# Kernel tuning notes

Measured on AMD Instinct MI355X. Metric: run time of the kernel, lower is better.

## Reference

```python
import jax, jax.numpy as jnp
import numpy as np
import math

B, T, H = 16, 2048, 128

def setup_inputs() -> dict:
    key = jax.random.key(0)
    kq, kk, kv = jax.random.split(key, 3)
    q = jax.random.normal(kq, (B, T, H), dtype=jnp.float32)
    k = jax.random.normal(kk, (B, T, H), dtype=jnp.float32)
    v = jax.random.normal(kv, (B, T, H), dtype=jnp.float32)
    # causal mask, shape (1,1,T,T) as in the torch module
    mask = jnp.tril(jnp.ones((T, T), dtype=jnp.int32))[None, None]
    return {"q": q, "k": k, "v": v, "mask": mask}

def reference(q, k, v, mask) -> jnp.ndarray:
    scale = math.sqrt(q.shape[-1])
    # (B,T,T) attention logits
    att = jnp.einsum("btd,bsd->bts", q, k) / scale
    m = mask[0, 0]  # (T,T), broadcasts over batch
    att = jnp.where(m == 0, -jnp.inf, att)
    att = jax.nn.softmax(att, axis=-1)
    # dropout is identity in eval mode (p=0.0)
    return jnp.einsum("bts,bsd->btd", att, v)
```

## Files before the change

kernel.cpp:

```cpp
#include <hip/hip_runtime.h>
#include <hip/hip_bf16.h>

#define TT 2048
#define DD 128
#define NB 16
#define NTILE 32
#define TILE_BYTES 16384

typedef __bf16 bf16x8 __attribute__((ext_vector_type(8)));
typedef __bf16 bf16x4 __attribute__((ext_vector_type(4)));
typedef float f32x4 __attribute__((ext_vector_type(4)));
typedef float f32x16 __attribute__((ext_vector_type(16)));

#define GLOAD_LDS16(g, l) __builtin_amdgcn_global_load_lds( \
    (const __attribute__((address_space(1))) void*)(g),     \
    (__attribute__((address_space(3))) void*)(l), 16, 0, 0)

__device__ __forceinline__ float warp16_sum(float v) {
    v += __shfl_xor(v, 1);
    v += __shfl_xor(v, 2);
    v += __shfl_xor(v, 4);
    v += __shfl_xor(v, 8);
    return v;
}
__device__ __forceinline__ float bf2f(unsigned int u16) {
    union { unsigned int i; float f; } x; x.i = u16 << 16; return x.f;
}
__device__ __forceinline__ unsigned int pk2(float lo, float hi) {
    unsigned short a = __builtin_bit_cast(unsigned short, (__bf16)lo);
    unsigned short b = __builtin_bit_cast(unsigned short, (__bf16)hi);
    return (unsigned int)a | ((unsigned int)b << 16);
}
__device__ __forceinline__ bf16x8 frag4(unsigned int a, unsigned int b,
                                        unsigned int c, unsigned int d) {
    uint4 u = make_uint4(a, b, c, d);
    return __builtin_bit_cast(bf16x8, u);
}
__device__ __forceinline__ f32x16 z16() {
    f32x16 v;
    #pragma unroll
    for (int i = 0; i < 16; ++i) v[i] = 0.f;
    return v;
}

__global__ __launch_bounds__(256) void prepass(
    const float* __restrict__ K, const float* __restrict__ V,
    char* __restrict__ KB, char* __restrict__ VTB)
{
    const int t = blockIdx.x;
    const int b = blockIdx.y;
    const int tid = threadIdx.x;
    char* kdst = KB  + (size_t)(b * NTILE + t) * TILE_BYTES;
    char* vdst = VTB + (size_t)(b * NTILE + t) * TILE_BYTES;
    const float* kp = K + ((size_t)b * TT + t * 64) * DD;
    const float* vp = V + ((size_t)b * TT + t * 64) * DD;

    #pragma unroll
    for (int it = 0; it < 4; ++it) {
        int key = it * 16 + (tid >> 4);
        int d0  = (tid & 15) * 8;
        const float4* s = (const float4*)(kp + (size_t)key * DD + d0);
        float4 f0 = s[0], f1 = s[1];
        bf16x8 h;
        h[0]=(__bf16)f0.x; h[1]=(__bf16)f0.y; h[2]=(__bf16)f0.z; h[3]=(__bf16)f0.w;
        h[4]=(__bf16)f1.x; h[5]=(__bf16)f1.y; h[6]=(__bf16)f1.z; h[7]=(__bf16)f1.w;
        *(bf16x8*)(kdst + key * 256 + ((d0 * 2) ^ ((key & 15) << 4))) = h;
    }
    #pragma unroll
    for (int it = 0; it < 4; ++it) {
        int d  = tid & 127;
        int k0 = ((tid >> 7) + it * 2) * 8;
        bf16x8 h;
        #pragma unroll
        for (int j = 0; j < 8; ++j)
            h[j] = (__bf16)vp[(size_t)(k0 + j) * DD + d];
        *(bf16x8*)(vdst + (d >> 1) * 256 +
                   ((((d & 1) * 128) + 2 * k0) ^ (((d >> 1) & 15) << 4))) = h;
    }
}

__global__ __launch_bounds__(256, 2) void attn_main(
    const float* __restrict__ Q,
    const char* __restrict__ KB, const char* __restrict__ VTB,
    float* __restrict__ O, char* __restrict__ SLOTS,
    int CHUNK, int NCMAX, int QBMIN)
{
    __shared__ __align__(16) unsigned short Klds[2][8192];
    __shared__ __align__(16) unsigned short Vs[2][8192];

    const int b  = blockIdx.x;
    const int qb = 15 - blockIdx.y;
    const int ntile = 2 * qb + 2;
    const int nc = (ntile + CHUNK - 1) / CHUNK;
    if ((int)blockIdx.z >= nc) return;
    const int t0 = (int)(((long)blockIdx.z * ntile) / nc);
    const int t1 = (int)(((long)(blockIdx.z + 1) * ntile) / nc);

    const int tid  = threadIdx.x;
    const int lane = tid & 63;
    const int w    = tid >> 6;
    const int ln   = lane & 31;
    const int hi   = lane >> 5;
    const int qrow0 = qb * 128 + w * 32;
    const int q_abs = qrow0 + ln;

    const float SCALE = 0.08838834764831845f;

    const float* qrow = Q + ((size_t)b * TT + q_abs) * DD + 8 * hi;
    bf16x8 qf[8];
    #pragma unroll
    for (int kc = 0; kc < 8; ++kc) {
        float4 f0 = *(const float4*)(qrow + kc * 16);
        float4 f1 = *(const float4*)(qrow + kc * 16 + 4);
        bf16x8 t;
        t[0]=(__bf16)f0.x; t[1]=(__bf16)f0.y; t[2]=(__bf16)f0.z; t[3]=(__bf16)f0.w;
        t[4]=(__bf16)f1.x; t[5]=(__bf16)f1.y; t[6]=(__bf16)f1.z; t[7]=(__bf16)f1.w;
        qf[kc] = t;
    }

    f32x16 o[4];
    #pragma unroll
    for (int dg = 0; dg < 4; ++dg) o[dg] = z16();
    float lsum = 0.f;

    const char* kbase = KB  + (size_t)b * NTILE * TILE_BYTES;
    const char* vbase = VTB + (size_t)b * NTILE * TILE_BYTES;

    auto STAGE = [&](int t, int buf) {
        const char* ks = kbase + (size_t)t * TILE_BYTES;
        const char* vs = vbase + (size_t)t * TILE_BYTES;
        #pragma unroll
        for (int j = 0; j < 4; ++j) {
            int off = (w * 4 + j) * 1024 + lane * 16;
            GLOAD_LDS16(ks + off, (char*)Klds[buf] + off);
            GLOAD_LDS16(vs + off, (char*)Vs[buf]  + off);
        }
    };

    STAGE(t0, 0);
    int cur = 0;

    for (int t = t0; t < t1; ++t) {
        const int kb = t * 64;
        __syncthreads();

        if (t + 1 < t1) STAGE(t + 1, cur ^ 1);

        if (kb <= qrow0 + 31) {
            const bool edge = (kb + 63 > qrow0);
            const char* kl = (const char*)Klds[cur];
            const char* vl = (const char*)Vs[cur];

            auto PROC = [&](int kg) {
                const int key = kg * 32 + ln;
                const int swk = (key & 15) << 4;
                const char* krow = kl + key * 256;
                f32x16 a0 = z16(), a1 = z16();
                #pragma unroll
                for (int kc = 0; kc < 8; kc += 2) {
                    bf16x8 kf0 = *(const bf16x8*)(krow + ((kc * 32 + 16 * hi) ^ swk));
                    bf16x8 kf1 = *(const bf16x8*)(krow + (((kc + 1) * 32 + 16 * hi) ^ swk));
                    a0 = __builtin_amdgcn_mfma_f32_32x32x16_bf16(kf0, qf[kc],     a0, 0, 0, 0);
                    a1 = __builtin_amdgcn_mfma_f32_32x32x16_bf16(kf1, qf[kc + 1], a1, 0, 0, 0);
                }
                float p[16];
                #pragma unroll
                for (int reg = 0; reg < 16; ++reg) {
                    int key_abs = kb + kg * 32 + (reg & 3) + 8 * (reg >> 2) + 4 * hi;
                    float pe = __expf((a0[reg] + a1[reg]) * SCALE);
                    if (edge && key_abs > q_abs) pe = 0.f;
                    p[reg] = pe;
                    lsum += pe;
                }
                unsigned int wd[8], xr[8];
                #pragma unroll
                for (int i = 0; i < 8; ++i) wd[i] = pk2(p[2 * i], p[2 * i + 1]);
                #pragma unroll
                for (int i = 0; i < 8; ++i) xr[i] = __shfl_xor(wd[i], 32);
                bf16x8 pa0 = hi ? frag4(xr[2], xr[3], wd[2], wd[3])
                                : frag4(wd[0], wd[1], xr[0], xr[1]);
                bf16x8 pa1 = hi ? frag4(xr[6], xr[7], wd[6], wd[7])
                                : frag4(wd[4], wd[5], xr[4], xr[5]);
                const int kc0 = 2 * kg;
                #pragma unroll
                for (int dg = 0; dg < 4; ++dg) {
                    int d = dg * 32 + ln;
                    const char* vrow = vl + (d >> 1) * 256;
                    int hv = (d & 1) * 128;
                    int swv = ((d >> 1) & 15) << 4;
                    bf16x8 vf0 = *(const bf16x8*)(vrow + ((hv + kc0 * 32 + 16 * hi) ^ swv));
                    bf16x8 vf1 = *(const bf16x8*)(vrow + ((hv + (kc0 + 1) * 32 + 16 * hi) ^ swv));
                    o[dg] = __builtin_amdgcn_mfma_f32_32x32x16_bf16(pa0, vf0, o[dg], 0, 0, 0);
                    o[dg] = __builtin_amdgcn_mfma_f32_32x32x16_bf16(pa1, vf1, o[dg], 0, 0, 0);
                }
            };

            PROC(0);
            if (kb + 32 <= qrow0 + 31) PROC(1);
        }
        cur ^= 1;
    }

    const float ltot = lsum + __shfl_xor(lsum, 32);

    if (t0 == 0 && t1 == ntile) {
        const float inv = 1.0f / ltot;
        float* op = O + ((size_t)b * TT + qrow0) * DD;
        #pragma unroll
        for (int reg = 0; reg < 16; ++reg) {
            int qr = (reg & 3) + 8 * (reg >> 2) + 4 * hi;
            float iv = __shfl(inv, qr);
            #pragma unroll
            for (int dg = 0; dg < 4; ++dg)
                op[(size_t)qr * DD + dg * 32 + ln] = o[dg][reg] * iv;
        }
    } else {
        const int NQ = 16 - QBMIN;
        char* slot = SLOTS + (size_t)((b * NQ + (qb - QBMIN)) * NCMAX + blockIdx.z) * 33280;
        unsigned short* so = (unsigned short*)slot;
        float* sl = (float*)(slot + 32768);
        #pragma unroll
        for (int reg = 0; reg < 16; ++reg) {
            int row = w * 32 + (reg & 3) + 8 * (reg >> 2) + 4 * hi;
            #pragma unroll
            for (int dg = 0; dg < 4; ++dg)
                so[row * 128 + dg * 32 + ln] =
                    __builtin_bit_cast(unsigned short, (__bf16)o[dg][reg]);
        }
        if (hi == 0) sl[w * 32 + ln] = ltot;
    }
}

__global__ __launch_bounds__(256) void attn_combine(
    const char* __restrict__ SLOTS, float* __restrict__ O,
    int CHUNK, int NCMAX, int QBMIN)
{
    const int qb = QBMIN + blockIdx.x;
    const int b  = blockIdx.y;
    const int nc = (2 * qb + 2 + CHUNK - 1) / CHUNK;
    const int NQ = 16 - QBMIN;
    const int row  = threadIdx.x >> 1;
    const int half = (threadIdx.x & 1) * 64;
    const char* base = SLOTS + (size_t)((b * NQ + (qb - QBMIN)) * NCMAX) * 33280;

    float l = 0.f;
    for (int c = 0; c < nc; ++c)
        l += *(const float*)(base + (size_t)c * 33280 + 32768 + row * 4);
    float inv = 1.0f / l;

    float* op = O + ((size_t)b * TT + qb * 128 + row) * DD + half;
    #pragma unroll
    for (int g = 0; g < 8; ++g) {
        f32x4 a0 = (f32x4){0.f,0.f,0.f,0.f}, a1 = (f32x4){0.f,0.f,0.f,0.f};
        for (int c = 0; c < nc; ++c) {
            const uint4 u = *(const uint4*)(base + (size_t)c * 33280 + row * 256 + half * 2 + g * 16);
            a0[0] += bf2f(u.x & 0xffffu); a0[1] += bf2f(u.x >> 16);
            a0[2] += bf2f(u.y & 0xffffu); a0[3] += bf2f(u.y >> 16);
            a1[0] += bf2f(u.z & 0xffffu); a1[1] += bf2f(u.z >> 16);
            a1[2] += bf2f(u.w & 0xffffu); a1[3] += bf2f(u.w >> 16);
        }
        float4 r0, r1;
        r0.x=a0[0]*inv; r0.y=a0[1]*inv; r0.z=a0[2]*inv; r0.w=a0[3]*inv;
        r1.x=a1[0]*inv; r1.y=a1[1]*inv; r1.z=a1[2]*inv; r1.w=a1[3]*inv;
        *(float4*)(op + g * 8)     = r0;
        *(float4*)(op + g * 8 + 4) = r1;
    }
}

__global__ __launch_bounds__(256) void attn_fb(
    const float* __restrict__ Q, const float* __restrict__ K,
    const float* __restrict__ V, float* __restrict__ O)
{
    __shared__ __align__(16) unsigned short Klds[2][64 * 128];
    __shared__ __align__(16) unsigned short Vsh[2][128 * 64];
    __shared__ __align__(16) unsigned short Plds[4][16 * 64];

    const int qb = 31 - blockIdx.x;
    const int b  = blockIdx.y;
    const int ntile = qb + 1;
    const int tid  = threadIdx.x;
    const int lane = tid & 63;
    const int w    = tid >> 6;
    const int x    = lane & 15;
    const int hi   = lane >> 4;
    const int qrow0 = qb * 64 + w * 16;

    const float* qp    = Q + ((size_t)b * TT + qrow0) * DD;
    const float* kbase = K + (size_t)b * TT * DD;
    const float* vbase = V + (size_t)b * TT * DD;
    const float SCALE = 0.08838834764831845f;

    const int krow = tid >> 5;
    const int d4   = (tid & 31) * 4;
    const int dd   = tid & 127;
    const int g    = tid >> 7;

    bf16x8 qf[4];
    #pragma unroll
    for (int kc = 0; kc < 4; ++kc) {
        const float4* s0 = (const float4*)(qp + x * DD + kc * 32 + 8 * hi);
        float4 f0 = s0[0], f1 = s0[1];
        bf16x8 t;
        t[0]=(__bf16)f0.x; t[1]=(__bf16)f0.y; t[2]=(__bf16)f0.z; t[3]=(__bf16)f0.w;
        t[4]=(__bf16)f1.x; t[5]=(__bf16)f1.y; t[6]=(__bf16)f1.z; t[7]=(__bf16)f1.w;
        qf[kc] = t;
    }
    f32x4 o[8];
    #pragma unroll
    for (int nt = 0; nt < 8; ++nt) o[nt] = (f32x4){0.f,0.f,0.f,0.f};
    float lsum[4] = {0.f,0.f,0.f,0.f};
    float4 kreg[8];
    float  vreg[32];

    auto LOAD = [&](int t) {
        const float* kp = kbase + (size_t)(t * 64) * DD;
        const float* vp = vbase + (size_t)(t * 64) * DD;
        #pragma unroll
        for (int it = 0; it < 8; ++it)
            kreg[it] = *(const float4*)(kp + (size_t)(it * 8 + krow) * DD + d4);
        #pragma unroll
        for (int j = 0; j < 32; ++j)
            vreg[j] = vp[(size_t)(g * 32 + j) * DD + dd];
    };
    auto WRITE = [&](int buf) {
        char* kb8 = (char*)Klds[buf];
        #pragma unroll
        for (int it = 0; it < 8; ++it) {
            int key = it * 8 + krow;
            float4 f = kreg[it];
            bf16x4 h;
            h[0]=(__bf16)f.x; h[1]=(__bf16)f.y; h[2]=(__bf16)f.z; h[3]=(__bf16)f.w;
            *(bf16x4*)(kb8 + key * 256 + ((d4 * 2) ^ ((key & 7) << 4))) = h;
        }
        char* vb8 = (char*)Vsh[buf];
        #pragma unroll
        for (int m4 = 0; m4 < 4; ++m4) {
            bf16x8 h;
            #pragma unroll
            for (int j = 0; j < 8; ++j) h[j] = (__bf16)vreg[m4 * 8 + j];
            *(bf16x8*)(vb8 + dd * 128 + ((g * 64 + m4 * 16) ^ ((dd & 7) << 4))) = h;
        }
    };

    LOAD(0); WRITE(0);
    int cur = 0;
    char* pmine = (char*)Plds[w];

    for (int t = 0; t < ntile; ++t) {
        const int kb = t * 64;
        __syncthreads();
        if (t + 1 < ntile) LOAD(t + 1);

        const bool diag  = (t == qb);
        const int  ntmax = diag ? w : 3;
        const char* kb8  = (const char*)Klds[cur];
        float p[4][4];
        #pragma unroll
        for (int nt = 0; nt < 4; ++nt) {
            int key = nt * 16 + x;
            if (nt <= ntmax) {
                f32x4 acc = (f32x4){0.f,0.f,0.f,0.f};
                #pragma unroll
                for (int kc = 0; kc < 4; ++kc) {
                    int off = key * 256 + ((kc * 64 + 16 * hi) ^ ((key & 7) << 4));
                    bf16x8 bfr = *(const bf16x8*)(kb8 + off);
                    acc = __builtin_amdgcn_mfma_f32_16x16x32_bf16(qf[kc], bfr, acc, 0, 0, 0);
                }
                #pragma unroll
                for (int r = 0; r < 4; ++r) {
                    bool msk = diag && (kb + key > qrow0 + 4 * hi + r);
                    float pe = msk ? 0.f : __expf(acc[r] * SCALE);
                    p[nt][r] = pe;
                    lsum[r] += pe;
                }
            } else {
                #pragma unroll
                for (int r = 0; r < 4; ++r) p[nt][r] = 0.f;
            }
        }
        #pragma unroll
        for (int nt = 0; nt < 4; ++nt)
            #pragma unroll
            for (int r = 0; r < 4; ++r) {
                int q = 4 * hi + r;
                *(unsigned short*)(pmine + q * 128 + (((nt * 16 + x) * 2) ^ ((q & 7) << 4))) =
                    __builtin_bit_cast(unsigned short, (__bf16)p[nt][r]);
            }
        const char* vb8 = (const char*)Vsh[cur];
        #pragma unroll
        for (int kc = 0; kc < 2; ++kc) {
            bf16x8 af = *(const bf16x8*)(pmine + x * 128 + ((kc * 64 + 16 * hi) ^ ((x & 7) << 4)));
            #pragma unroll
            for (int nt = 0; nt < 8; ++nt) {
                int d = nt * 16 + x;
                bf16x8 bfr = *(const bf16x8*)(vb8 + d * 128 + ((kc * 64 + 16 * hi) ^ ((d & 7) << 4)));
                o[nt] = __builtin_amdgcn_mfma_f32_16x16x32_bf16(af, bfr, o[nt], 0, 0, 0);
            }
        }
        if (t + 1 < ntile) WRITE(cur ^ 1);
        cur ^= 1;
    }
    float* op = O + ((size_t)b * TT + qrow0) * DD;
    #pragma unroll
    for (int r = 0; r < 4; ++r) {
        float lr = warp16_sum(lsum[r]);
        float inv = 1.0f / lr;
        #pragma unroll
        for (int nt = 0; nt < 8; ++nt)
            op[(size_t)(4 * hi + r) * DD + nt * 16 + x] = o[nt][r] * inv;
    }
}

extern "C" void kernel_launch(void* const* d_in, const int* in_sizes, int n_in,
                              void* d_out, int out_size, void* d_ws, size_t ws_size,
                              hipStream_t stream) {
    const float* q = (const float*)d_in[0];
    const float* k = (const float*)d_in[1];
    const float* v = (const float*)d_in[2];
    float* out = (float*)d_out;

    const size_t PRE = (size_t)2 * NB * NTILE * TILE_BYTES;
    auto slotsNeed = [](int QBMIN, int NCMAX) {
        return (size_t)(16 - QBMIN) * NB * NCMAX * 33280;
    };

    char* kb  = (char*)d_ws;
    char* vtb = kb + (size_t)NB * NTILE * TILE_BYTES;
    char* slots = vtb + (size_t)NB * NTILE * TILE_BYTES;

    if (ws_size >= PRE + slotsNeed(4, 4)) {
        prepass<<<dim3(NTILE, NB), 256, 0, stream>>>(k, v, kb, vtb);
        attn_main<<<dim3(NB, 16, 4), 256, 0, stream>>>(q, kb, vtb, out, slots, 8, 4, 4);
        attn_combine<<<dim3(12, NB), 256, 0, stream>>>(slots, out, 8, 4, 4);
    } else if (ws_size >= PRE + slotsNeed(8, 2)) {
        prepass<<<dim3(NTILE, NB), 256, 0, stream>>>(k, v, kb, vtb);
        attn_main<<<dim3(NB, 16, 2), 256, 0, stream>>>(q, kb, vtb, out, slots, 16, 2, 8);
        attn_combine<<<dim3(8, NB), 256, 0, stream>>>(slots, out, 16, 2, 8);
    } else if (ws_size >= PRE) {
        prepass<<<dim3(NTILE, NB), 256, 0, stream>>>(k, v, kb, vtb);
        attn_main<<<dim3(NB, 16, 1), 256, 0, stream>>>(q, kb, vtb, out, slots, 32, 1, 16);
    } else {
        attn_fb<<<dim3(32, NB), 256, 0, stream>>>(q, k, v, out);
    }
}
```

Before: 76.04 us.

## Halve KV tile to 32 keys, rebalance split-K chunks with compact slot layout

Shrinks the KV tile from 64 to 32 keys, changing the prepass layout, LDS staging and the per-tile compute to a single 32-key group. Split-K chunking now uses 12 tiles per chunk with up to 6 chunks and a compact per-batch slot offset table, so more query blocks get split and the causal tail wastes less work. It also adds s_setprio around the MFMA sections. In exchange there are twice as many barrier and tile iterations, each with less MFMA work to hide latency.

Result: slower. 86.50 us (+13.8%).

```diff
diff --git a/kernel.cpp b/kernel.cpp
--- a/kernel.cpp
+++ b/kernel.cpp
@@ -4,8 +4,9 @@
 #define TT 2048
 #define DD 128
 #define NB 16
-#define NTILE 32
-#define TILE_BYTES 16384
+#define KVB 32
+#define NTILE 64
+#define TILE_BYTES 8192
 
 typedef __bf16 bf16x8 __attribute__((ext_vector_type(8)));
 typedef __bf16 bf16x4 __attribute__((ext_vector_type(4)));
@@ -41,6 +42,9 @@
     #pragma unroll
     for (int i = 0; i < 16; ++i) v[i] = 0.f;
     return v;
+}
+__device__ __forceinline__ int ncof(int qb, int C) {
+    return (4 * qb + 4 + C - 1) / C;
 }
 
 __global__ __launch_bounds__(256) void prepass(
@@ -52,11 +56,11 @@
     const int tid = threadIdx.x;
     char* kdst = KB  + (size_t)(b * NTILE + t) * TILE_BYTES;
     char* vdst = VTB + (size_t)(b * NTILE + t) * TILE_BYTES;
-    const float* kp = K + ((size_t)b * TT + t * 64) * DD;
-    const float* vp = V + ((size_t)b * TT + t * 64) * DD;
-
-    #pragma unroll
-    for (int it = 0; it < 4; ++it) {
+    const float* kp = K + ((size_t)b * TT + t * KVB) * DD;
+    const float* vp = V + ((size_t)b * TT + t * KVB) * DD;
+
+    #pragma unroll
+    for (int it = 0; it < 2; ++it) {
         int key = it * 16 + (tid >> 4);
         int d0  = (tid & 15) * 8;
         const float4* s = (const float4*)(kp + (size_t)key * DD + d0);
@@ -67,15 +71,15 @@
         *(bf16x8*)(kdst + key * 256 + ((d0 * 2) ^ ((key & 15) << 4))) = h;
     }
     #pragma unroll
-    for (int it = 0; it < 4; ++it) {
+    for (int it = 0; it < 2; ++it) {
         int d  = tid & 127;
         int k0 = ((tid >> 7) + it * 2) * 8;
         bf16x8 h;
         #pragma unroll
         for (int j = 0; j < 8; ++j)
             h[j] = (__bf16)vp[(size_t)(k0 + j) * DD + d];
-        *(bf16x8*)(vdst + (d >> 1) * 256 +
-                   ((((d & 1) * 128) + 2 * k0) ^ (((d >> 1) & 15) << 4))) = h;
+        *(bf16x8*)(vdst + (d >> 2) * 256 +
+                   (((d & 3) * 64 + 2 * k0) ^ (((d >> 2) & 15) << 4))) = h;
     }
 }
 
@@ -83,15 +87,15 @@
     const float* __restrict__ Q,
     const char* __restrict__ KB, const char* __restrict__ VTB,
     float* __restrict__ O, char* __restrict__ SLOTS,
-    int CHUNK, int NCMAX, int QBMIN)
+    int CHUNK, int SLOTS_PER_B)
 {
-    __shared__ __align__(16) unsigned short Klds[2][8192];
-    __shared__ __align__(16) unsigned short Vs[2][8192];
+    __shared__ __align__(16) unsigned short Klds[2][4096];
+    __shared__ __align__(16) unsigned short Vs[2][4096];
 
     const int b  = blockIdx.x;
     const int qb = 15 - blockIdx.y;
-    const int ntile = 2 * qb + 2;
-    const int nc = (ntile + CHUNK - 1) / CHUNK;
+    const int ntile = 4 * qb + 4;
+    const int nc = ncof(qb, CHUNK);
     if ((int)blockIdx.z >= nc) return;
     const int t0 = (int)(((long)blockIdx.z * ntile) / nc);
     const int t1 = (int)(((long)(blockIdx.z + 1) * ntile) / nc);
@@ -130,8 +134,8 @@
         const char* ks = kbase + (size_t)t * TILE_BYTES;
         const char* vs = vbase + (size_t)t * TILE_BYTES;
         #pragma unroll
-        for (int j = 0; j < 4; ++j) {
-            int off = (w * 4 + j) * 1024 + lane * 16;
+        for (int j = 0; j < 2; ++j) {
+            int off = (w + j * 4) * 1024 + lane * 16;
             GLOAD_LDS16(ks + off, (char*)Klds[buf] + off);
             GLOAD_LDS16(vs + off, (char*)Vs[buf]  + off);
         }
@@ -141,69 +145,68 @@
     int cur = 0;
 
     for (int t = t0; t < t1; ++t) {
-        const int kb = t * 64;
+        const int kb = t * KVB;
         __syncthreads();
 
         if (t + 1 < t1) STAGE(t + 1, cur ^ 1);
 
         if (kb <= qrow0 + 31) {
-            const bool edge = (kb + 63 > qrow0);
+            const bool edge = (kb + 31 > qrow0);
             const char* kl = (const char*)Klds[cur];
             const char* vl = (const char*)Vs[cur];
 
-            auto PROC = [&](int kg) {
-                const int key = kg * 32 + ln;
-                const int swk = (key & 15) << 4;
-                const char* krow = kl + key * 256;
-                f32x16 a0 = z16(), a1 = z16();
-                #pragma unroll
-                for (int kc = 0; kc < 8; kc += 2) {
-                    bf16x8 kf0 = *(const bf16x8*)(krow + ((kc * 32 + 16 * hi) ^ swk));
-                    bf16x8 kf1 = *(const bf16x8*)(krow + (((kc + 1) * 32 + 16 * hi) ^ swk));
-                    a0 = __builtin_amdgcn_mfma_f32_32x32x16_bf16(kf0, qf[kc],     a0, 0, 0, 0);
-                    a1 = __builtin_amdgcn_mfma_f32_32x32x16_bf16(kf1, qf[kc + 1], a1, 0, 0, 0);
-                }
-                float p[16];
-                #pragma unroll
-                for (int reg = 0; reg < 16; ++reg) {
-                    int key_abs = kb + kg * 32 + (reg & 3) + 8 * (reg >> 2) + 4 * hi;
-                    float pe = __expf((a0[reg] + a1[reg]) * SCALE);
-                    if (edge && key_abs > q_abs) pe = 0.f;
-                    p[reg] = pe;
-                    lsum += pe;
-                }
-                unsigned int wd[8], xr[8];
-                #pragma unroll
-                for (int i = 0; i < 8; ++i) wd[i] = pk2(p[2 * i], p[2 * i + 1]);
-                #pragma unroll
-                for (int i = 0; i < 8; ++i) xr[i] = __shfl_xor(wd[i], 32);
-                bf16x8 pa0 = hi ? frag4(xr[2], xr[3], wd[2], wd[3])
-                                : frag4(wd[0], wd[1], xr[0], xr[1]);
-                bf16x8 pa1 = hi ? frag4(xr[6], xr[7], wd[6], wd[7])
-                                : frag4(wd[4], wd[5], xr[4], xr[5]);
-                const int kc0 = 2 * kg;
-                #pragma unroll
-                for (int dg = 0; dg < 4; ++dg) {
-                    int d = dg * 32 + ln;
-                    const char* vrow = vl + (d >> 1) * 256;
-                    int hv = (d & 1) * 128;
-                    int swv = ((d >> 1) & 15) << 4;
-                    bf16x8 vf0 = *(const bf16x8*)(vrow + ((hv + kc0 * 32 + 16 * hi) ^ swv));
-                    bf16x8 vf1 = *(const bf16x8*)(vrow + ((hv + (kc0 + 1) * 32 + 16 * hi) ^ swv));
-                    o[dg] = __builtin_amdgcn_mfma_f32_32x32x16_bf16(pa0, vf0, o[dg], 0, 0, 0);
-                    o[dg] = __builtin_amdgcn_mfma_f32_32x32x16_bf16(pa1, vf1, o[dg], 0, 0, 0);
-                }
-            };
-
-            PROC(0);
-            if (kb + 32 <= qrow0 + 31) PROC(1);
+            const int swk = (ln & 15) << 4;
+            const char* krow = kl + ln * 256;
+            f32x16 a0 = z16(), a1 = z16();
+            __builtin_amdgcn_s_setprio(1);
+            #pragma unroll
+            for (int kc = 0; kc < 8; kc += 2) {
+                bf16x8 kf0 = *(const bf16x8*)(krow + ((kc * 32 + 16 * hi) ^ swk));
+                bf16x8 kf1 = *(const bf16x8*)(krow + (((kc + 1) * 32 + 16 * hi) ^ swk));
+                a0 = __builtin_amdgcn_mfma_f32_32x32x16_bf16(kf0, qf[kc],     a0, 0, 0, 0);
+                a1 = __builtin_amdgcn_mfma_f32_32x32x16_bf16(kf1, qf[kc + 1], a1, 0, 0, 0);
+            }
+            __builtin_amdgcn_s_setprio(0);
+            float p[16];
+            float ls0 = 0.f, ls1 = 0.f;
+            #pragma unroll
+            for (int reg = 0; reg < 16; ++reg) {
+                int key_abs = kb + (reg & 3) + 8 * (reg >> 2) + 4 * hi;
+                float pe = __expf((a0[reg] + a1[reg]) * SCALE);
+                if (edge && key_abs > q_abs) pe = 0.f;
+                p[reg] = pe;
+                if (reg & 1) ls1 += pe; else ls0 += pe;
+            }
+            lsum += ls0 + ls1;
+            unsigned int wd[8], xr[8];
+            #pragma unroll
+            for (int i = 0; i < 8; ++i) wd[i] = pk2(p[2 * i], p[2 * i + 1]);
+            #pragma unroll
+            for (int i = 0; i < 8; ++i) xr[i] = __shfl_xor(wd[i], 32);
+            bf16x8 pa0 = hi ? frag4(xr[2], xr[3], wd[2], wd[3])
+                            : frag4(wd[0], wd[1], xr[0], xr[1]);
+            bf16x8 pa1 = hi ? frag4(xr[6], xr[7], wd[6], wd[7])
+                            : frag4(wd[4], wd[5], xr[4], xr[5]);
+            __builtin_amdgcn_s_setprio(1);
+            #pragma unroll
+            for (int dg = 0; dg < 4; ++dg) {
+                int d = dg * 32 + ln;
+                const char* vrow = vl + (d >> 2) * 256;
+                int base = (d & 3) * 64;
+                int swv = ((d >> 2) & 15) << 4;
+                bf16x8 vf0 = *(const bf16x8*)(vrow + ((base + 16 * hi) ^ swv));
+                bf16x8 vf1 = *(const bf16x8*)(vrow + ((base + 32 + 16 * hi) ^ swv));
+                o[dg] = __builtin_amdgcn_mfma_f32_32x32x16_bf16(pa0, vf0, o[dg], 0, 0, 0);
+                o[dg] = __builtin_amdgcn_mfma_f32_32x32x16_bf16(pa1, vf1, o[dg], 0, 0, 0);
+            }
+            __builtin_amdgcn_s_setprio(0);
         }
         cur ^= 1;
     }
 
     const float ltot = lsum + __shfl_xor(lsum, 32);
 
-    if (t0 == 0 && t1 == ntile) {
+    if (nc == 1) {
         const float inv = 1.0f / ltot;
         float* op = O + ((size_t)b * TT + qrow0) * DD;
         #pragma unroll
@@ -215,8 +218,12 @@
                 op[(size_t)qr * DD + dg * 32 + ln] = o[dg][reg] * iv;
         }
     } else {
-        const int NQ = 16 - QBMIN;
-        char* slot = SLOTS + (size_t)((b * NQ + (qb - QBMIN)) * NCMAX + blockIdx.z) * 33280;
+        int off = 0;
+        for (int q = 0; q < qb; ++q) {
+            int c = ncof(q, CHUNK);
+            if (c >= 2) off += c;
+        }
+        char* slot = SLOTS + (size_t)(b * SLOTS_PER_B + off + blockIdx.z) * 33280;
         unsigned short* so = (unsigned short*)slot;
         float* sl = (float*)(slot + 32768);
         #pragma unroll
@@ -233,15 +240,20 @@
 
 __global__ __launch_bounds__(256) void attn_combine(
     const char* __restrict__ SLOTS, float* __restrict__ O,
-    int CHUNK, int NCMAX, int QBMIN)
+    int CHUNK, int SLOTS_PER_B)
 {
-    const int qb = QBMIN + blockIdx.x;
+    const int qb = blockIdx.x;
     const int b  = blockIdx.y;
-    const int nc = (2 * qb + 2 + CHUNK - 1) / CHUNK;
-    const int NQ = 16 - QBMIN;
+    const int nc = ncof(qb, CHUNK);
+    if (nc < 2) return;
+    int off = 0;
+    for (int q = 0; q < qb; ++q) {
+        int c = ncof(q, CHUNK);
+        if (c >= 2) off += c;
+    }
     const int row  = threadIdx.x >> 1;
     const int half = (threadIdx.x & 1) * 64;
-    const char* base = SLOTS + (size_t)((b * NQ + (qb - QBMIN)) * NCMAX) * 33280;
+    const char* base = SLOTS + (size_t)(b * SLOTS_PER_B + off) * 33280;
 
     float l = 0.f;
     for (int c = 0; c < nc; ++c)
@@ -420,25 +432,33 @@
     float* out = (float*)d_out;
 
     const size_t PRE = (size_t)2 * NB * NTILE * TILE_BYTES;
-    auto slotsNeed = [](int QBMIN, int NCMAX) {
-        return (size_t)(16 - QBMIN) * NB * NCMAX * 33280;
+    auto slotsPerB = [](int C) {
+        int s = 0;
+        for (int qb = 0; qb < 16; ++qb) {
+            int nc = (4 * qb + 4 + C - 1) / C;
+            if (nc >= 2) s += nc;
+        }
+        return s;
     };
 
     char* kb  = (char*)d_ws;
     char* vtb = kb + (size_t)NB * NTILE * TILE_BYTES;
     char* slots = vtb + (size_t)NB * NTILE * TILE_BYTES;
 
-    if (ws_size >= PRE + slotsNeed(4, 4)) {
+    const int spb12 = slotsPerB(12);
+    const int spb16 = slotsPerB(16);
+
+    if (ws_size >= PRE + (size_t)NB * spb12 * 33280) {
         prepass<<<dim3(NTILE, NB), 256, 0, stream>>>(k, v, kb, vtb);
-        attn_main<<<dim3(NB, 16, 4), 256, 0, stream>>>(q, kb, vtb, out, slots, 8, 4, 4);
-        attn_combine<<<dim3(12, NB), 256, 0, stream>>>(slots, out, 8, 4, 4);
-    } else if (ws_size >= PRE + slotsNeed(8, 2)) {
+        attn_main<<<dim3(NB, 16, 6), 256, 0, stream>>>(q, kb, vtb, out, slots, 12, spb12);
+        attn_combine<<<dim3(16, NB), 256, 0, stream>>>(slots, out, 12, spb12);
+    } else if (ws_size >= PRE + (size_t)NB * spb16 * 33280) {
         prepass<<<dim3(NTILE, NB), 256, 0, stream>>>(k, v, kb, vtb);
-        attn_main<<<dim3(NB, 16, 2), 256, 0, stream>>>(q, kb, vtb, out, slots, 16, 2, 8);
-        attn_combine<<<dim3(8, NB), 256, 0, stream>>>(slots, out, 16, 2, 8);
+        attn_main<<<dim3(NB, 16, 4), 256, 0, stream>>>(q, kb, vtb, out, slots, 16, spb16);
+        attn_combine<<<dim3(16, NB), 256, 0, stream>>>(slots, out, 16, spb16);
     } else if (ws_size >= PRE) {
         prepass<<<dim3(NTILE, NB), 256, 0, stream>>>(k, v, kb, vtb);
-        attn_main<<<dim3(NB, 16, 1), 256, 0, stream>>>(q, kb, vtb, out, slots, 32, 1, 16);
+        attn_main<<<dim3(NB, 16, 1), 256, 0, stream>>>(q, kb, vtb, out, slots, 64, 0);
     } else {
         attn_fb<<<dim3(32, NB), 256, 0, stream>>>(q, k, v, out);
     }
```
